# Optimization experiments

Measured on AMD Instinct MI355X. Metric: run time of the kernel, lower is better.

## Reference

```python
import jax, jax.numpy as jnp
import numpy as np
import math

D_MODEL = 768
N_HEADS = 6
HD = D_MODEL // N_HEADS  # 128
RANK = D_MODEL // 4      # 192
B, T = 128, 256


def _rope_tables(T, dim):
    # matches torch: inv = 1/10000**(arange(0,dim,2)/dim); emb = cat([outer(t,inv)]*2, -1)
    inv = 1.0 / (10000.0 ** (jnp.arange(0, dim, 2, dtype=jnp.float32) / dim))
    t = jnp.arange(T, dtype=jnp.float32)
    freqs = jnp.outer(t, inv)                       # [T, dim/2]
    emb = jnp.concatenate([freqs, freqs], axis=-1)  # [T, dim]
    return jnp.cos(emb), jnp.sin(emb)               # each [T, dim]


def _rot(x):
    h = x.shape[-1] // 2
    return jnp.concatenate([-x[..., h:], x[..., :h]], axis=-1)


def setup_inputs() -> dict:
    key = jax.random.key(0)
    ks = jax.random.split(key, 8)
    s_in = 1.0 / math.sqrt(D_MODEL)
    s_r = 1.0 / math.sqrt(RANK)
    inp = {
        'x': jax.random.normal(ks[0], (B, T, D_MODEL), dtype=jnp.float32),
        'qA': jax.random.normal(ks[1], (D_MODEL, RANK), dtype=jnp.float32) * s_in,
        'qB': jax.random.normal(ks[2], (RANK, D_MODEL), dtype=jnp.float32) * s_r,
        'kA': jax.random.normal(ks[3], (D_MODEL, RANK), dtype=jnp.float32) * s_in,
        'kB': jax.random.normal(ks[4], (RANK, D_MODEL), dtype=jnp.float32) * s_r,
        'vA': jax.random.normal(ks[5], (D_MODEL, RANK), dtype=jnp.float32) * s_in,
        'vB': jax.random.normal(ks[6], (RANK, D_MODEL), dtype=jnp.float32) * s_r,
        'o_w': jax.random.normal(ks[7], (D_MODEL, D_MODEL), dtype=jnp.float32) * s_in,
    }
    return inp


def reference(x, qA, qB, kA, kB, vA, vB, o_w):
    Bb, Tt, _ = x.shape
    # low-rank projections: in -> rank -> out, then split heads [B, H, T, hd]
    def proj(A, W):
        h = (x @ A) @ W
        return h.reshape(Bb, Tt, N_HEADS, HD).transpose(0, 2, 1, 3)
    q = proj(qA, qB)
    k = proj(kA, kB)
    v = proj(vA, vB)
    cos, sin = _rope_tables(Tt, HD)  # [T, hd], broadcast over B, H
    q = q * cos + _rot(q) * sin
    k = k * cos + _rot(k) * sin
    att = jnp.einsum('bhqd,bhkd->bhqk', q, k) / math.sqrt(HD)
    causal = jnp.tril(jnp.ones((Tt, Tt), dtype=bool))
    att = jnp.where(causal, att, -jnp.inf)
    att = jax.nn.softmax(att, axis=-1)
    out = jnp.einsum('bhqk,bhkd->bhqd', att, v)          # [B, H, T, hd]
    out = out.transpose(0, 2, 1, 3).reshape(Bb, Tt, D_MODEL)
    return out @ o_w
```

## Files before the change

### kernel.cpp

```cpp
#include <hip/hip_runtime.h>
#include <hip/hip_bf16.h>
#include <stdint.h>

typedef __attribute__((ext_vector_type(8))) short s16x8;
typedef __attribute__((ext_vector_type(4))) float f32x4;

#define D_MODEL 768
#define N_HEADS 6
#define HD 128
#define RANK 192
#define TT 256
#define NROW 32768
#define QKV_LD 2304
#define NK 12

__device__ inline short f2bf(float f) {
  union { float f; unsigned u; } x; x.f = f;
  unsigned r = x.u + 0x7fffu + ((x.u >> 16) & 1u);
  return (short)(r >> 16);
}
__device__ inline float bf2f(short v) {
  union { unsigned u; float f; } x; x.u = ((unsigned)(unsigned short)v) << 16;
  return x.f;
}
__device__ inline void gload_lds16(const void* g, void* lds) {
  __builtin_amdgcn_global_load_lds(
      (const __attribute__((address_space(1))) unsigned int*)g,
      (__attribute__((address_space(3))) unsigned int*)lds, 16, 0, 0);
}

#define BAR()    asm volatile("s_barrier" ::: "memory")
#define LGKM0()  asm volatile("s_waitcnt lgkmcnt(0)" ::: "memory")
#define WAITVM4() asm volatile("s_waitcnt vmcnt(4)" ::: "memory")
#define WAITVM0() asm volatile("s_waitcnt vmcnt(0)" ::: "memory")

__global__ void k_tables(float* __restrict__ cosT, float* __restrict__ sinT) {
  int tid = blockIdx.x * 256 + threadIdx.x;
  int t = tid >> 6, i = tid & 63;
  float inv = powf(10000.0f, -(float)i / 64.0f);
  float ang = (float)t * inv;
  cosT[tid] = cosf(ang);
  sinT[tid] = sinf(ang);
}

__global__ void k_castx(const float* __restrict__ x, short* __restrict__ xb) {
  int t = blockIdx.x * 256 + threadIdx.x;
  const float4* xp = (const float4*)x;
  float4 a = xp[t * 2], b = xp[t * 2 + 1];
  s16x8 o;
  o[0] = f2bf(a.x); o[1] = f2bf(a.y); o[2] = f2bf(a.z); o[3] = f2bf(a.w);
  o[4] = f2bf(b.x); o[5] = f2bf(b.y); o[6] = f2bf(b.z); o[7] = f2bf(b.w);
  *(s16x8*)(xb + (size_t)t * 8) = o;
}

__global__ void k_makew(const float* __restrict__ qA, const float* __restrict__ qB,
                        const float* __restrict__ kA, const float* __restrict__ kB,
                        const float* __restrict__ vA, const float* __restrict__ vB,
                        short* __restrict__ WT) {
  int g = blockIdx.x * 256 + threadIdx.x;
  int n = g % 2304, kkb = g / 2304;
  int part = n / 768, nn = n % 768;
  const float* A = (part == 0) ? qA : (part == 1) ? kA : vA;
  const float* Bm = (part == 0) ? qB : (part == 1) ? kB : vB;
  float acc0 = 0.f, acc1 = 0.f, acc2 = 0.f, acc3 = 0.f;
  for (int r = 0; r < RANK; ++r) {
    float bv = Bm[r * 768 + nn];
    acc0 += A[(kkb + 0 * 192) * RANK + r] * bv;
    acc1 += A[(kkb + 1 * 192) * RANK + r] * bv;
    acc2 += A[(kkb + 2 * 192) * RANK + r] * bv;
    acc3 += A[(kkb + 3 * 192) * RANK + r] * bv;
  }
  WT[(size_t)n * 768 + kkb + 0 * 192] = f2bf(acc0);
  WT[(size_t)n * 768 + kkb + 1 * 192] = f2bf(acc1);
  WT[(size_t)n * 768 + kkb + 2 * 192] = f2bf(acc2);
  WT[(size_t)n * 768 + kkb + 3 * 192] = f2bf(acc3);
}

__global__ void k_wot(const float* __restrict__ ow, short* __restrict__ WT) {
  int g = blockIdx.x * 256 + threadIdx.x;
  int n = g % 768, kk = g / 768;
  WT[(size_t)(2304 + n) * 768 + kk] = f2bf(ow[(size_t)kk * 768 + n]);
}

__device__ inline s16x8 rdfrag(const short* hbase, int rowbyte, int ksl4x, int swz) {
  return *(const s16x8*)((const char*)hbase + rowbyte + (((ksl4x) ^ (swz)) << 4));
}

template <bool OUTBF>
__global__ __launch_bounds__(512, 2) void k_gemm8(const short* __restrict__ A,
                                                  const short* __restrict__ Bt,
                                                  void* __restrict__ Cv, int ldc) {
  extern __shared__ short lds[];
  const int tid = threadIdx.x;
  const int wid = tid >> 6, lane = tid & 63;
  const int l15 = lane & 15, l4 = lane >> 4;
  const int wr = wid >> 2, wc = wid & 3;
  const int swz = l15 & 7;
  const long mbase = (long)blockIdx.x * 256;
  const long nbase = (long)blockIdx.y * 256;

  const int hb0 = wid * 2048 + lane * 16;
  const int hb1 = hb0 + 1024;
  const int r0 = hb0 >> 7, c0 = ((hb0 >> 4) & 7) ^ (r0 & 7);
  const int r1 = hb1 >> 7, c1 = ((hb1 >> 4) & 7) ^ (r1 & 7);
  const int off0 = r0 * 768 + c0 * 8;
  const int off1 = r1 * 768 + c1 * 8;

#define STAGE(G, rowoff, kt, ldsS) do {                                        \
    gload_lds16((G) + (size_t)(rowoff) * 768 + (kt) * 64 + off0,               \
                (char*)(ldsS) + wid * 2048);                                   \
    gload_lds16((G) + (size_t)(rowoff) * 768 + (kt) * 64 + off1,               \
                (char*)(ldsS) + wid * 2048 + 1024);                            \
  } while (0)

#define LDSA(buf, half) (lds + ((buf) * 2 + (half)) * 8192)
#define LDSB(buf, half) (lds + 32768 + ((buf) * 2 + (half)) * 8192)

  f32x4 acc[8][4] = {};

  STAGE(A,  mbase,       0, LDSA(0, 0));
  STAGE(Bt, nbase,       0, LDSB(0, 0));
  STAGE(A,  mbase + 128, 0, LDSA(0, 1));
  STAGE(Bt, nbase + 128, 0, LDSB(0, 1));
  STAGE(A,  mbase,       1, LDSA(1, 0));
  STAGE(Bt, nbase,       1, LDSB(1, 0));
  WAITVM4();
  BAR();

  s16x8 a03[4][2], a47[4][2], b01[2][2], b23[2][2];

#pragma unroll
  for (int kt = 0; kt < NK; ++kt) {
    const int buf = kt & 1, nbuf = buf ^ 1;
    const short* Ab = LDSA(buf, wr);
    const short* Bb = LDSB(buf, (wc >> 1));
    const int browbase = (wc & 1) * 64 * 128;

#pragma unroll
    for (int mf = 0; mf < 4; ++mf)
#pragma unroll
      for (int ks = 0; ks < 2; ++ks)
        a03[mf][ks] = rdfrag(Ab, (mf * 16 + l15) * 128, ks * 4 + l4, swz);
#pragma unroll
    for (int nf = 0; nf < 2; ++nf)
#pragma unroll
      for (int ks = 0; ks < 2; ++ks)
        b01[nf][ks] = rdfrag(Bb, browbase + (nf * 16 + l15) * 128, ks * 4 + l4, swz);
    if (kt + 1 < NK) STAGE(A, mbase + 128, kt + 1, LDSA(nbuf, 1));
    BAR();
    LGKM0();
    __builtin_amdgcn_s_setprio(1);
#pragma unroll
    for (int mf = 0; mf < 4; ++mf)
#pragma unroll
      for (int nf = 0; nf < 2; ++nf)
#pragma unroll
        for (int ks = 0; ks < 2; ++ks)
          acc[mf][nf] = __builtin_amdgcn_mfma_f32_16x16x32_bf16(a03[mf][ks], b01[nf][ks], acc[mf][nf], 0, 0, 0);
    __builtin_amdgcn_s_setprio(0);
    BAR();

#pragma unroll
    for (int mf = 0; mf < 4; ++mf)
#pragma unroll
      for (int ks = 0; ks < 2; ++ks)
        a47[mf][ks] = rdfrag(Ab, ((mf + 4) * 16 + l15) * 128, ks * 4 + l4, swz);
    if (kt + 1 < NK) STAGE(Bt, nbase + 128, kt + 1, LDSB(nbuf, 1));
    BAR();
    LGKM0();
    __builtin_amdgcn_s_setprio(1);
#pragma unroll
    for (int mf = 0; mf < 4; ++mf)
#pragma unroll
      for (int nf = 0; nf < 2; ++nf)
#pragma unroll
        for (int ks = 0; ks < 2; ++ks)
          acc[mf + 4][nf] = __builtin_amdgcn_mfma_f32_16x16x32_bf16(a47[mf][ks], b01[nf][ks], acc[mf + 4][nf], 0, 0, 0);
    __builtin_amdgcn_s_setprio(0);
    BAR();

#pragma unroll
    for (int nf = 0; nf < 2; ++nf)
#pragma unroll
      for (int ks = 0; ks < 2; ++ks)
        b23[nf][ks] = rdfrag(Bb, browbase + ((nf + 2) * 16 + l15) * 128, ks * 4 + l4, swz);
    if (kt + 2 < NK) STAGE(A, mbase, kt + 2, LDSA(buf, 0));
    BAR();
    LGKM0();
    __builtin_amdgcn_s_setprio(1);
#pragma unroll
    for (int mf = 0; mf < 4; ++mf)
#pragma unroll
      for (int nf = 0; nf < 2; ++nf)
#pragma unroll
        for (int ks = 0; ks < 2; ++ks)
          acc[mf][nf + 2] = __builtin_amdgcn_mfma_f32_16x16x32_bf16(a03[mf][ks], b23[nf][ks], acc[mf][nf + 2], 0, 0, 0);
    __builtin_amdgcn_s_setprio(0);
    BAR();

    if (kt + 2 < NK) STAGE(Bt, nbase, kt + 2, LDSB(buf, 0));
    BAR();
    __builtin_amdgcn_s_setprio(1);
#pragma unroll
    for (int mf = 0; mf < 4; ++mf)
#pragma unroll
      for (int nf = 0; nf < 2; ++nf)
#pragma unroll
        for (int ks = 0; ks < 2; ++ks)
          acc[mf + 4][nf + 2] = __builtin_amdgcn_mfma_f32_16x16x32_bf16(a47[mf][ks], b23[nf][ks], acc[mf + 4][nf + 2], 0, 0, 0);
    __builtin_amdgcn_s_setprio(0);
    if (kt < NK - 1) {
      if (kt + 2 < NK) WAITVM4(); else WAITVM0();
      BAR();
    }
  }
#undef STAGE

#pragma unroll
  for (int mf = 0; mf < 8; ++mf)
#pragma unroll
    for (int nf = 0; nf < 4; ++nf)
#pragma unroll
      for (int r = 0; r < 4; ++r) {
        long row = mbase + wr * 128 + mf * 16 + l4 * 4 + r;
        long col = nbase + wc * 64 + nf * 16 + l15;
        if (OUTBF) ((short*)Cv)[row * ldc + col] = f2bf(acc[mf][nf][r]);
        else       ((float*)Cv)[row * ldc + col] = acc[mf][nf][r];
      }
}

__global__ void k_rope8(short* __restrict__ qkv, const float* __restrict__ cosT,
                        const float* __restrict__ sinT) {
  int tid = blockIdx.x * 256 + threadIdx.x;
  int row = tid / 96, rem = tid % 96;
  int part = rem / 48, rem2 = rem % 48;
  int head = rem2 >> 3, i8 = (rem2 & 7) * 8;
  int t = row & (TT - 1);
  size_t base = (size_t)row * QKV_LD + part * 768 + head * 128 + i8;
  s16x8 a = *(const s16x8*)(qkv + base);
  s16x8 b = *(const s16x8*)(qkv + base + 64);
  const float4* cp = (const float4*)(cosT + t * 64 + i8);
  const float4* sp = (const float4*)(sinT + t * 64 + i8);
  float4 c04 = cp[0], c14 = cp[1], s04 = sp[0], s14 = sp[1];
  float cs[8] = {c04.x, c04.y, c04.z, c04.w, c14.x, c14.y, c14.z, c14.w};
  float sn[8] = {s04.x, s04.y, s04.z, s04.w, s14.x, s14.y, s14.z, s14.w};
  float scale = (part == 0) ? 0.08838834764831845f : 1.0f;
  s16x8 na, nb;
#pragma unroll
  for (int j = 0; j < 8; ++j) {
    float av = bf2f(a[j]), bv = bf2f(b[j]);
    na[j] = f2bf((av * cs[j] - bv * sn[j]) * scale);
    nb[j] = f2bf((bv * cs[j] + av * sn[j]) * scale);
  }
  *(s16x8*)(qkv + base) = na;
  *(s16x8*)(qkv + base + 64) = nb;
}

__global__ __launch_bounds__(512) void k_attn(const short* __restrict__ qkv,
                                              short* __restrict__ attout) {
  __shared__ short Kls[64 * 128];
  __shared__ short Vls[64 * 128];
  __shared__ short Pls[8][32 * 64];
  const int tid = threadIdx.x;
  const int wid = tid >> 6, lane = tid & 63;
  const int l15 = lane & 15, l4 = lane >> 4;
  const int b = blockIdx.x / N_HEADS, h = blockIdx.x % N_HEADS;
  const long row0 = (long)b * TT;

  s16x8 qf[2][4];
#pragma unroll
  for (int mi = 0; mi < 2; ++mi)
#pragma unroll
    for (int kc = 0; kc < 4; ++kc) {
      long row = row0 + wid * 32 + mi * 16 + l15;
      qf[mi][kc] = *(const s16x8*)(qkv + row * QKV_LD + h * HD + kc * 32 + l4 * 8);
    }

  float mst[2][4], lst[2][4];
  f32x4 oacc[2][8];
#pragma unroll
  for (int mi = 0; mi < 2; ++mi)
#pragma unroll
    for (int r = 0; r < 4; ++r) { mst[mi][r] = -1e30f; lst[mi][r] = 0.f; }
#pragma unroll
  for (int mi = 0; mi < 2; ++mi)
#pragma unroll
    for (int nd = 0; nd < 8; ++nd) oacc[mi][nd] = {0.f, 0.f, 0.f, 0.f};

  const int jmax = (wid * 32 + 31) / 64;
  for (int j = 0; j < 4; ++j) {
#pragma unroll
    for (int q2 = 0; q2 < 2; ++q2) {
      int off = wid * 2048 + q2 * 1024;
      int si = (off >> 1) + lane * 8;
      int kv = si >> 7, d = si & 127;
      long grow = row0 + j * 64 + kv;
      gload_lds16(qkv + grow * QKV_LD + D_MODEL + h * HD + d, (char*)Kls + off);
      gload_lds16(qkv + grow * QKV_LD + 2 * D_MODEL + h * HD + d, (char*)Vls + off);
    }
    __syncthreads();
    if (j <= jmax) {
      f32x4 sacc[2][4] = {};
#pragma unroll
      for (int kc = 0; kc < 4; ++kc) {
        s16x8 kf[4];
#pragma unroll
        for (int ni = 0; ni < 4; ++ni)
          kf[ni] = *(const s16x8*)(Kls + (ni * 16 + l15) * 128 + kc * 32 + l4 * 8);
#pragma unroll
        for (int mi = 0; mi < 2; ++mi)
#pragma unroll
          for (int ni = 0; ni < 4; ++ni)
            sacc[mi][ni] = __builtin_amdgcn_mfma_f32_16x16x32_bf16(qf[mi][kc], kf[ni], sacc[mi][ni], 0, 0, 0);
      }
#pragma unroll
      for (int mi = 0; mi < 2; ++mi) {
#pragma unroll
        for (int r = 0; r < 4; ++r) {
          int qr = wid * 32 + mi * 16 + l4 * 4 + r;
          float rm = -1e30f;
#pragma unroll
          for (int ni = 0; ni < 4; ++ni) {
            int kvc = j * 64 + ni * 16 + l15;
            if (kvc > qr) sacc[mi][ni][r] = -1e30f;
            rm = fmaxf(rm, sacc[mi][ni][r]);
          }
#pragma unroll
          for (int d2 = 1; d2 < 16; d2 <<= 1)
            rm = fmaxf(rm, __shfl_xor(rm, d2, 64));
          float mold = mst[mi][r];
          float mnew = fmaxf(mold, rm);
          float alpha = __expf(mold - mnew);
          mst[mi][r] = mnew;
          float rs = 0.f;
#pragma unroll
          for (int ni = 0; ni < 4; ++ni) {
            float p = __expf(sacc[mi][ni][r] - mnew);
            sacc[mi][ni][r] = p;
            rs += p;
          }
#pragma unroll
          for (int d2 = 1; d2 < 16; d2 <<= 1)
            rs += __shfl_xor(rs, d2, 64);
          lst[mi][r] = lst[mi][r] * alpha + rs;
#pragma unroll
          for (int nd = 0; nd < 8; ++nd)
            oacc[mi][nd][r] *= alpha;
        }
      }
#pragma unroll
      for (int mi = 0; mi < 2; ++mi)
#pragma unroll
        for (int ni = 0; ni < 4; ++ni)
#pragma unroll
          for (int r = 0; r < 4; ++r)
            Pls[wid][(mi * 16 + l4 * 4 + r) * 64 + ni * 16 + l15] = f2bf(sacc[mi][ni][r]);
      asm volatile("s_waitcnt lgkmcnt(0)" ::: "memory");
      __builtin_amdgcn_sched_barrier(0);
#pragma unroll
      for (int kc2 = 0; kc2 < 2; ++kc2) {
        s16x8 pa[2];
#pragma unroll
        for (int mi = 0; mi < 2; ++mi)
          pa[mi] = *(const s16x8*)(&Pls[wid][(mi * 16 + l15) * 64 + kc2 * 32 + l4 * 8]);
#pragma unroll
        for (int nd = 0; nd < 8; ++nd) {
          s16x8 vf;
#pragma unroll
          for (int jj = 0; jj < 8; ++jj)
            vf[jj] = Vls[(kc2 * 32 + l4 * 8 + jj) * 128 + nd * 16 + l15];
#pragma unroll
          for (int mi = 0; mi < 2; ++mi)
            oacc[mi][nd] = __builtin_amdgcn_mfma_f32_16x16x32_bf16(pa[mi], vf, oacc[mi][nd], 0, 0, 0);
        }
      }
    }
    __syncthreads();
  }
#pragma unroll
  for (int mi = 0; mi < 2; ++mi)
#pragma unroll
    for (int nd = 0; nd < 8; ++nd)
#pragma unroll
      for (int r = 0; r < 4; ++r) {
        long row = row0 + wid * 32 + mi * 16 + l4 * 4 + r;
        int col = h * HD + nd * 16 + l15;
        attout[row * D_MODEL + col] = f2bf(oacc[mi][nd][r] / lst[mi][r]);
      }
}

extern "C" void kernel_launch(void* const* d_in, const int* in_sizes, int n_in,
                              void* d_out, int out_size, void* d_ws, size_t ws_size,
                              hipStream_t stream) {
  const float* x  = (const float*)d_in[0];
  const float* qA = (const float*)d_in[1];
  const float* qB = (const float*)d_in[2];
  const float* kA = (const float*)d_in[3];
  const float* kB = (const float*)d_in[4];
  const float* vA = (const float*)d_in[5];
  const float* vB = (const float*)d_in[6];
  const float* ow = (const float*)d_in[7];

  char* ws = (char*)d_ws;
  short* qkv   = (short*)ws;
  short* xb    = (short*)(ws + 150994944);
  short* WT    = (short*)(ws + 201326592);
  float* cosT  = (float*)(ws + 206045184);
  float* sinT  = (float*)(ws + 206110720);
  short* attout = xb;

  hipFuncSetAttribute((const void*)k_gemm8<true>,
                      hipFuncAttributeMaxDynamicSharedMemorySize, 131072);
  hipFuncSetAttribute((const void*)k_gemm8<false>,
                      hipFuncAttributeMaxDynamicSharedMemorySize, 131072);

  k_tables<<<64, 256, 0, stream>>>(cosT, sinT);
  k_castx<<<12288, 256, 0, stream>>>(x, xb);
  k_makew<<<1728, 256, 0, stream>>>(qA, qB, kA, kB, vA, vB, WT);
  k_wot<<<2304, 256, 0, stream>>>(ow, WT);
  k_gemm8<true><<<dim3(128, 9), 512, 131072, stream>>>(xb, WT, (void*)qkv, QKV_LD);
  k_rope8<<<12288, 256, 0, stream>>>(qkv, cosT, sinT);
  k_attn<<<768, 512, 0, stream>>>(qkv, attout);
  k_gemm8<false><<<dim3(128, 3), 512, 131072, stream>>>(attout, WT + (size_t)2304 * 768, d_out, 768);
}
```

Before: 412.9 us.

## Fuse Q rope into attention, swizzle K/V/P LDS, transpose V, register-tile makew

Several unrelated changes land together. makew now computes a 4x4 output tile per thread with float4 loads. The GEMM remaps block IDs so consecutive blocks are spread across XCD chiplets. Q RoPE and its scale move into the attention kernel's register prologue, so the standalone rope pass only touches K and does half the traffic. Inside attention, K and P use XOR-swizzled LDS layouts and V is stored transposed, replacing eight scalar LDS reads per fragment with one vector read; this adds an extra barrier per KV tile and scalar LDS writes for the transpose.

```diff
diff --git a/kernel.cpp b/kernel.cpp
--- a/kernel.cpp
+++ b/kernel.cpp
@@ -13,6 +13,7 @@
 #define NROW 32768
 #define QKV_LD 2304
 #define NK 12
+#define QSCL 0.08838834764831845f
 
 __device__ inline short f2bf(float f) {
   union { float f; unsigned u; } x; x.f = f;
@@ -58,22 +59,36 @@
                         const float* __restrict__ vA, const float* __restrict__ vB,
                         short* __restrict__ WT) {
   int g = blockIdx.x * 256 + threadIdx.x;
-  int n = g % 2304, kkb = g / 2304;
-  int part = n / 768, nn = n % 768;
+  int n4 = g % 576, kkb = g / 576;
+  int part = n4 / 192, nnb = (n4 % 192) * 4;
   const float* A = (part == 0) ? qA : (part == 1) ? kA : vA;
   const float* Bm = (part == 0) ? qB : (part == 1) ? kB : vB;
-  float acc0 = 0.f, acc1 = 0.f, acc2 = 0.f, acc3 = 0.f;
-  for (int r = 0; r < RANK; ++r) {
-    float bv = Bm[r * 768 + nn];
-    acc0 += A[(kkb + 0 * 192) * RANK + r] * bv;
-    acc1 += A[(kkb + 1 * 192) * RANK + r] * bv;
-    acc2 += A[(kkb + 2 * 192) * RANK + r] * bv;
-    acc3 += A[(kkb + 3 * 192) * RANK + r] * bv;
+  float acc[4][4] = {};
+  for (int r0 = 0; r0 < RANK; r0 += 4) {
+    float4 a4[4], b4[4];
+#pragma unroll
+    for (int q = 0; q < 4; ++q)
+      a4[q] = *(const float4*)&A[(kkb + q * 192) * RANK + r0];
+#pragma unroll
+    for (int i = 0; i < 4; ++i)
+      b4[i] = *(const float4*)&Bm[(r0 + i) * 768 + nnb];
+#pragma unroll
+    for (int q = 0; q < 4; ++q) {
+      const float* aq = (const float*)&a4[q];
+#pragma unroll
+      for (int i = 0; i < 4; ++i) {
+        const float* bi = (const float*)&b4[i];
+#pragma unroll
+        for (int jn = 0; jn < 4; ++jn)
+          acc[q][jn] += aq[i] * bi[jn];
+      }
+    }
   }
-  WT[(size_t)n * 768 + kkb + 0 * 192] = f2bf(acc0);
-  WT[(size_t)n * 768 + kkb + 1 * 192] = f2bf(acc1);
-  WT[(size_t)n * 768 + kkb + 2 * 192] = f2bf(acc2);
-  WT[(size_t)n * 768 + kkb + 3 * 192] = f2bf(acc3);
+#pragma unroll
+  for (int q = 0; q < 4; ++q)
+#pragma unroll
+    for (int jn = 0; jn < 4; ++jn)
+      WT[(size_t)(part * 768 + nnb + jn) * 768 + kkb + q * 192] = f2bf(acc[q][jn]);
 }
 
 __global__ void k_wot(const float* __restrict__ ow, short* __restrict__ WT) {
@@ -96,8 +111,11 @@
   const int l15 = lane & 15, l4 = lane >> 4;
   const int wr = wid >> 2, wc = wid & 3;
   const int swz = l15 & 7;
-  const long mbase = (long)blockIdx.x * 256;
-  const long nbase = (long)blockIdx.y * 256;
+  const int bid = blockIdx.y * 128 + blockIdx.x;
+  const int cpx = (gridDim.y * 128) >> 3;
+  const int sbid = (bid & 7) * cpx + (bid >> 3);
+  const long mbase = (long)(sbid & 127) * 256;
+  const long nbase = (long)(sbid >> 7) * 256;
 
   const int hb0 = wid * 2048 + lane * 16;
   const int hb1 = hb0 + 1024;
@@ -229,14 +247,13 @@
       }
 }
 
-__global__ void k_rope8(short* __restrict__ qkv, const float* __restrict__ cosT,
+__global__ void k_ropek(short* __restrict__ qkv, const float* __restrict__ cosT,
                         const float* __restrict__ sinT) {
   int tid = blockIdx.x * 256 + threadIdx.x;
-  int row = tid / 96, rem = tid % 96;
-  int part = rem / 48, rem2 = rem % 48;
-  int head = rem2 >> 3, i8 = (rem2 & 7) * 8;
+  int row = tid / 48, rem = tid % 48;
+  int head = rem >> 3, i8 = (rem & 7) * 8;
   int t = row & (TT - 1);
-  size_t base = (size_t)row * QKV_LD + part * 768 + head * 128 + i8;
+  size_t base = (size_t)row * QKV_LD + D_MODEL + head * 128 + i8;
   s16x8 a = *(const s16x8*)(qkv + base);
   s16x8 b = *(const s16x8*)(qkv + base + 64);
   const float4* cp = (const float4*)(cosT + t * 64 + i8);
@@ -244,22 +261,23 @@
   float4 c04 = cp[0], c14 = cp[1], s04 = sp[0], s14 = sp[1];
   float cs[8] = {c04.x, c04.y, c04.z, c04.w, c14.x, c14.y, c14.z, c14.w};
   float sn[8] = {s04.x, s04.y, s04.z, s04.w, s14.x, s14.y, s14.z, s14.w};
-  float scale = (part == 0) ? 0.08838834764831845f : 1.0f;
   s16x8 na, nb;
 #pragma unroll
   for (int j = 0; j < 8; ++j) {
     float av = bf2f(a[j]), bv = bf2f(b[j]);
-    na[j] = f2bf((av * cs[j] - bv * sn[j]) * scale);
-    nb[j] = f2bf((bv * cs[j] + av * sn[j]) * scale);
+    na[j] = f2bf(av * cs[j] - bv * sn[j]);
+    nb[j] = f2bf(bv * cs[j] + av * sn[j]);
   }
   *(s16x8*)(qkv + base) = na;
   *(s16x8*)(qkv + base + 64) = nb;
 }
 
 __global__ __launch_bounds__(512) void k_attn(const short* __restrict__ qkv,
-                                              short* __restrict__ attout) {
+                                              short* __restrict__ attout,
+                                              const float* __restrict__ cosT,
+                                              const float* __restrict__ sinT) {
   __shared__ short Kls[64 * 128];
-  __shared__ short Vls[64 * 128];
+  __shared__ short Vt[128 * 64];
   __shared__ short Pls[8][32 * 64];
   const int tid = threadIdx.x;
   const int wid = tid >> 6, lane = tid & 63;
@@ -275,6 +293,25 @@
       long row = row0 + wid * 32 + mi * 16 + l15;
       qf[mi][kc] = *(const s16x8*)(qkv + row * QKV_LD + h * HD + kc * 32 + l4 * 8);
     }
+#pragma unroll
+  for (int mi = 0; mi < 2; ++mi) {
+    int t = wid * 32 + mi * 16 + l15;
+#pragma unroll
+    for (int kc = 0; kc < 2; ++kc) {
+      const float4* cp = (const float4*)(cosT + t * 64 + kc * 32 + l4 * 8);
+      const float4* sp = (const float4*)(sinT + t * 64 + kc * 32 + l4 * 8);
+      float4 c04 = cp[0], c14 = cp[1], s04 = sp[0], s14 = sp[1];
+      float cs[8] = {c04.x, c04.y, c04.z, c04.w, c14.x, c14.y, c14.z, c14.w};
+      float sn[8] = {s04.x, s04.y, s04.z, s04.w, s14.x, s14.y, s14.z, s14.w};
+#pragma unroll
+      for (int jj = 0; jj < 8; ++jj) {
+        float av = bf2f(qf[mi][kc][jj]);
+        float bv = bf2f(qf[mi][kc + 2][jj]);
+        qf[mi][kc][jj]     = f2bf((av * cs[jj] - bv * sn[jj]) * QSCL);
+        qf[mi][kc + 2][jj] = f2bf((bv * cs[jj] + av * sn[jj]) * QSCL);
+      }
+    }
+  }
 
   float mst[2][4], lst[2][4];
   f32x4 oacc[2][8];
@@ -288,17 +325,28 @@
     for (int nd = 0; nd < 8; ++nd) oacc[mi][nd] = {0.f, 0.f, 0.f, 0.f};
 
   const int jmax = (wid * 32 + 31) / 64;
+  const int d0 = wid * 16;
   for (int j = 0; j < 4; ++j) {
 #pragma unroll
     for (int q2 = 0; q2 < 2; ++q2) {
-      int off = wid * 2048 + q2 * 1024;
-      int si = (off >> 1) + lane * 8;
-      int kv = si >> 7, d = si & 127;
-      long grow = row0 + j * 64 + kv;
-      gload_lds16(qkv + grow * QKV_LD + D_MODEL + h * HD + d, (char*)Kls + off);
-      gload_lds16(qkv + grow * QKV_LD + 2 * D_MODEL + h * HD + d, (char*)Vls + off);
-    }
+      int bb = wid * 2048 + q2 * 1024 + lane * 16;
+      int r = bb >> 8;
+      int cpos = (bb >> 4) & 15;
+      int sc = cpos ^ (r & 7);
+      gload_lds16(qkv + (row0 + j * 64 + r) * QKV_LD + D_MODEL + h * HD + sc * 8,
+                  (char*)Kls + wid * 2048 + q2 * 1024);
+    }
+    const short* vsrc = qkv + (row0 + j * 64 + lane) * QKV_LD + 2 * D_MODEL + h * HD + d0;
+    s16x8 v0 = *(const s16x8*)vsrc;
+    s16x8 v1 = *(const s16x8*)(vsrc + 8);
     __syncthreads();
+#pragma unroll
+    for (int e = 0; e < 8; ++e)
+      *(short*)((char*)Vt + (d0 + e) * 128 + (((lane >> 3) ^ e) << 4) + (lane & 7) * 2) = v0[e];
+#pragma unroll
+    for (int e = 0; e < 8; ++e)
+      *(short*)((char*)Vt + (d0 + 8 + e) * 128 + (((lane >> 3) ^ e) << 4) + (lane & 7) * 2) = v1[e];
+
     if (j <= jmax) {
       f32x4 sacc[2][4] = {};
 #pragma unroll
@@ -306,7 +354,8 @@
         s16x8 kf[4];
 #pragma unroll
         for (int ni = 0; ni < 4; ++ni)
-          kf[ni] = *(const s16x8*)(Kls + (ni * 16 + l15) * 128 + kc * 32 + l4 * 8);
+          kf[ni] = *(const s16x8*)((const char*)Kls + (ni * 16 + l15) * 256 +
+                                   (((kc * 4 + l4) ^ (l15 & 7)) << 4));
 #pragma unroll
         for (int mi = 0; mi < 2; ++mi)
 #pragma unroll
@@ -353,22 +402,27 @@
 #pragma unroll
         for (int ni = 0; ni < 4; ++ni)
 #pragma unroll
-          for (int r = 0; r < 4; ++r)
-            Pls[wid][(mi * 16 + l4 * 4 + r) * 64 + ni * 16 + l15] = f2bf(sacc[mi][ni][r]);
-      asm volatile("s_waitcnt lgkmcnt(0)" ::: "memory");
-      __builtin_amdgcn_sched_barrier(0);
+          for (int r = 0; r < 4; ++r) {
+            int prow = mi * 16 + l4 * 4 + r;
+            int pcp = (ni * 2 + (l15 >> 3)) ^ (prow & 7);
+            *(short*)((char*)Pls[wid] + prow * 128 + (pcp << 4) + (l15 & 7) * 2) =
+                f2bf(sacc[mi][ni][r]);
+          }
+    }
+    LGKM0();
+    BAR();
+    if (j <= jmax) {
 #pragma unroll
       for (int kc2 = 0; kc2 < 2; ++kc2) {
         s16x8 pa[2];
 #pragma unroll
         for (int mi = 0; mi < 2; ++mi)
-          pa[mi] = *(const s16x8*)(&Pls[wid][(mi * 16 + l15) * 64 + kc2 * 32 + l4 * 8]);
+          pa[mi] = *(const s16x8*)((const char*)Pls[wid] + (mi * 16 + l15) * 128 +
+                                   (((kc2 * 4 + l4) ^ (l15 & 7)) << 4));
 #pragma unroll
         for (int nd = 0; nd < 8; ++nd) {
-          s16x8 vf;
-#pragma unroll
-          for (int jj = 0; jj < 8; ++jj)
-            vf[jj] = Vls[(kc2 * 32 + l4 * 8 + jj) * 128 + nd * 16 + l15];
+          s16x8 vf = *(const s16x8*)((const char*)Vt + (nd * 16 + l15) * 128 +
+                                     (((kc2 * 4 + l4) ^ (l15 & 7)) << 4));
 #pragma unroll
           for (int mi = 0; mi < 2; ++mi)
             oacc[mi][nd] = __builtin_amdgcn_mfma_f32_16x16x32_bf16(pa[mi], vf, oacc[mi][nd], 0, 0, 0);
@@ -416,10 +470,10 @@
 
   k_tables<<<64, 256, 0, stream>>>(cosT, sinT);
   k_castx<<<12288, 256, 0, stream>>>(x, xb);
-  k_makew<<<1728, 256, 0, stream>>>(qA, qB, kA, kB, vA, vB, WT);
+  k_makew<<<432, 256, 0, stream>>>(qA, qB, kA, kB, vA, vB, WT);
   k_wot<<<2304, 256, 0, stream>>>(ow, WT);
   k_gemm8<true><<<dim3(128, 9), 512, 131072, stream>>>(xb, WT, (void*)qkv, QKV_LD);
-  k_rope8<<<12288, 256, 0, stream>>>(qkv, cosT, sinT);
-  k_attn<<<768, 512, 0, stream>>>(qkv, attout);
+  k_ropek<<<6144, 256, 0, stream>>>(qkv, cosT, sinT);
+  k_attn<<<768, 512, 0, stream>>>(qkv, attout, cosT, sinT);
   k_gemm8<false><<<dim3(128, 3), 512, 131072, stream>>>(attout, WT + (size_t)2304 * 768, d_out, 768);
 }
```

Measured after the change: 383.8 us. -7.0%, faster.
